# Optimization experiments

Measured on AMD Instinct MI355X. Metric: run time of the kernel, lower is better.

The kernel has to match this reference:

```python
import jax, jax.numpy as jnp
import numpy as np

V, D, NL = 50257, 768, 12
DI, DS, DC, DTR = 1536, 16, 4, 48  # d_inner, d_state, d_conv, dt_rank
B, S = 2, 1024


def _mamba_layer(x, iw, cw, cb, xw, dw, db, Alog, Dp, ow):
    # x: (B,S,D)
    xz = x @ iw.T                      # (B,S,2*DI)
    xin, z = jnp.split(xz, 2, axis=-1)
    # depthwise causal conv over sequence
    xc = jax.lax.conv_general_dilated(
        jnp.transpose(xin, (0, 2, 1)), cw[:, None, :],
        window_strides=(1,), padding=[(DC - 1, 0)],
        feature_group_count=DI, dimension_numbers=('NCL', 'OIL', 'NCL'))
    xin = jax.nn.silu(jnp.transpose(xc, (0, 2, 1)) + cb)  # (B,S,DI)
    dbl = xin @ xw.T                   # (B,S,DTR+2*DS)
    dt, Bm, Cm = dbl[..., :DTR], dbl[..., DTR:DTR + DS], dbl[..., DTR + DS:]
    dt = jax.nn.softplus(dt @ dw.T + db)  # (B,S,DI)
    A = -jnp.exp(Alog)                 # (DI,DS)

    def step(h, inp):
        dt_t, B_t, C_t, x_t = inp      # (B,DI),(B,DS),(B,DS),(B,DI)
        h = h * jnp.exp(dt_t[:, :, None] * A) + (dt_t * x_t)[:, :, None] * B_t[:, None, :]
        y = jnp.einsum('bds,bs->bd', h, C_t)
        return h, y

    h0 = jnp.zeros((x.shape[0], DI, DS), dtype=x.dtype)
    xs = (jnp.transpose(dt, (1, 0, 2)), jnp.transpose(Bm, (1, 0, 2)),
          jnp.transpose(Cm, (1, 0, 2)), jnp.transpose(xin, (1, 0, 2)))
    _, ys = jax.lax.scan(step, h0, xs)
    y = jnp.transpose(ys, (1, 0, 2)) + xin * Dp  # (B,S,DI)
    y = y * jax.nn.silu(z)
    return y @ ow.T                    # (B,S,D)


def _layernorm(x, w, b):
    mu = jnp.mean(x, axis=-1, keepdims=True)
    var = jnp.mean(jnp.square(x - mu), axis=-1, keepdims=True)
    return (x - mu) * jax.lax.rsqrt(var + 1e-5) * w + b


def setup_inputs() -> dict:
    key = jax.random.key(0)
    ks = jax.random.split(key, 10)
    s = 0.02
    input_ids = jax.random.randint(ks[0], (B, S), 0, V)
    emb = jax.random.normal(ks[1], (V, D), jnp.float32) * s
    in_proj_w = jax.random.normal(ks[2], (NL, 2 * DI, D), jnp.float32) * s
    conv_w = jax.random.normal(ks[3], (NL, DI, DC), jnp.float32) * 0.2
    conv_b = jnp.zeros((NL, DI), jnp.float32)
    x_proj_w = jax.random.normal(ks[4], (NL, DTR + 2 * DS, DI), jnp.float32) * s
    dt_proj_w = jax.random.normal(ks[5], (NL, DI, DTR), jnp.float32) * (DTR ** -0.5)
    dt_proj_b = jax.random.normal(ks[6], (NL, DI), jnp.float32) * 0.1 - 4.0
    A_log = jnp.broadcast_to(jnp.log(jnp.arange(1, DS + 1, dtype=jnp.float32)), (NL, DI, DS)) + 0.0
    D_param = jnp.ones((NL, DI), jnp.float32)
    out_proj_w = jax.random.normal(ks[7], (NL, D, DI), jnp.float32) * s
    norm_w = jnp.ones((D,), jnp.float32)
    norm_b = jnp.zeros((D,), jnp.float32)
    return {"input_ids": input_ids, "emb": emb, "in_proj_w": in_proj_w,
            "conv_w": conv_w, "conv_b": conv_b, "x_proj_w": x_proj_w,
            "dt_proj_w": dt_proj_w, "dt_proj_b": dt_proj_b, "A_log": A_log,
            "D_param": D_param, "out_proj_w": out_proj_w,
            "norm_w": norm_w, "norm_b": norm_b}


def reference(input_ids, emb, in_proj_w, conv_w, conv_b, x_proj_w, dt_proj_w,
              dt_proj_b, A_log, D_param, out_proj_w, norm_w, norm_b):
    x = emb[input_ids] * (D ** 0.5)    # (B,S,D)
    for i in range(NL):
        x = _mamba_layer(x, in_proj_w[i], conv_w[i], conv_b[i], x_proj_w[i],
                         dt_proj_w[i], dt_proj_b[i], A_log[i], D_param[i], out_proj_w[i])
    x = _layernorm(x, norm_w, norm_b)
    return x @ emb.T                   # tied lm_head: (B,S,V)
```

## Files before the change

### kernel.cpp

```cpp
#include <hip/hip_runtime.h>
#include <hip/hip_bf16.h>

#define DI 1536
#define DS 16
#define DC 4
#define DTR 48
#define NB 2
#define SL 1024
#define DM 768
#define NLAYER 12
#define VOCAB 50257
#define ROWS (NB*SL)
#define CCH 32
#define CLEN (SL/CCH)
#define NBIG (DI+32)

typedef __attribute__((ext_vector_type(8))) short bf16x8;
typedef __attribute__((ext_vector_type(4))) short short4v;
typedef __attribute__((ext_vector_type(4))) float f32x4;

__device__ inline short f2bf(float f) {
    unsigned u = __builtin_bit_cast(unsigned, f);
    unsigned r = (u + 0x7fffu + ((u >> 16) & 1u)) >> 16;
    return (short)r;
}
__device__ inline float bf2f(unsigned short u) {
    unsigned x = ((unsigned)u) << 16;
    return __builtin_bit_cast(float, x);
}

__device__ __forceinline__ void gl_lds16(const void* g, void* l) {
    __builtin_amdgcn_global_load_lds(
        (const __attribute__((address_space(1))) unsigned int*)g,
        (__attribute__((address_space(3))) unsigned int*)l, 16, 0, 0);
}

__global__ __launch_bounds__(256) void cvt_bf16_k(const float* __restrict__ src,
                                                  unsigned short* __restrict__ dst,
                                                  int n4) {
    int i = blockIdx.x * 256 + threadIdx.x;
    if (i >= n4) return;
    float4 v = *reinterpret_cast<const float4*>(src + (size_t)i * 4);
    short4v o;
    o[0] = f2bf(v.x); o[1] = f2bf(v.y); o[2] = f2bf(v.z); o[3] = f2bf(v.w);
    *reinterpret_cast<short4v*>(dst + (size_t)i * 4) = o;
}

__global__ __launch_bounds__(256) void wc_k(
    const float* __restrict__ dtw_all,
    const float* __restrict__ xpw_all,
    unsigned short* __restrict__ wbig)
{
    int l = blockIdx.z;
    const float* dtw = dtw_all + (size_t)l * DI * DTR;
    const float* xpw = xpw_all + (size_t)l * 80 * DI;
    unsigned short* wb = wbig + (size_t)l * NBIG * DI;
    int tid = threadIdx.x;
    if (blockIdx.y == 12) {
        if (blockIdx.x == 0) {
            for (int idx = tid; idx < 32 * DI; idx += 256) {
                int rr = idx / DI, k = idx - rr * DI;
                wb[(size_t)(DI + rr) * DI + k] =
                    (unsigned short)f2bf(xpw[(size_t)(48 + rr) * DI + k]);
            }
        }
        return;
    }
    __shared__ float sd[128 * 48];
    __shared__ float sx[48 * 128];
    int d0 = blockIdx.y * 128, k0 = blockIdx.x * 128;
    for (int idx = tid; idx < 128 * 48; idx += 256) {
        int r = idx / 48, j = idx - r * 48;
        sd[idx] = dtw[(size_t)(d0 + r) * DTR + j];
    }
    for (int idx = tid; idx < 48 * 128; idx += 256) {
        int j = idx / 128, k = idx - j * 128;
        sx[idx] = xpw[(size_t)j * DI + k0 + k];
    }
    __syncthreads();
    int tx = tid & 15, ty = tid >> 4;
    float acc[8][8] = {};
    for (int j = 0; j < 48; ++j) {
        float a[8], w[8];
        #pragma unroll
        for (int i = 0; i < 8; ++i) a[i] = sd[(ty * 8 + i) * 48 + j];
        #pragma unroll
        for (int i = 0; i < 8; ++i) w[i] = sx[j * 128 + tx * 8 + i];
        #pragma unroll
        for (int i = 0; i < 8; ++i)
            #pragma unroll
            for (int jj = 0; jj < 8; ++jj)
                acc[i][jj] += a[i] * w[jj];
    }
    for (int i = 0; i < 8; ++i)
        for (int jj = 0; jj < 8; ++jj)
            wb[(size_t)(d0 + ty * 8 + i) * DI + k0 + tx * 8 + jj] =
                (unsigned short)f2bf(acc[i][jj]);
}

__global__ __launch_bounds__(256) void embed_k(const int* __restrict__ ids,
                                               const float* __restrict__ emb,
                                               unsigned short* __restrict__ xbf) {
    int i = blockIdx.x * 256 + threadIdx.x;
    if (i >= ROWS * DM) return;
    int row = i / DM;
    int c = i - row * DM;
    xbf[i] = (unsigned short)f2bf(emb[(size_t)ids[row] * DM + c] * 27.712812921102035f);
}

template<int MT, int OUT, bool NTST>
__global__ __launch_bounds__(256) void gemm_bf16(
    const unsigned short* __restrict__ A, int lda,
    const unsigned short* __restrict__ W, int ldw,
    float* __restrict__ C, unsigned short* __restrict__ Cbf, int ldc,
    int GY, int N, int K,
    const float* __restrict__ bias, float* __restrict__ aux)
{
    constexpr int BKT = 32;
    constexpr int CPR = BKT / 8;
    constexpr int ACA = MT * CPR / 256;
    constexpr int ACW = 128 * CPR / 256;
    constexpr int ISS = ACA + ACW;
    constexpr int MFR = MT / 32;
    constexpr int BUFS = (MT + 128) * BKT;
    __shared__ __align__(16) short smem[2 * BUFS];

    const int tid  = threadIdx.x;
    const int lane = tid & 63;
    const int wid  = tid >> 6;
    const int wr   = wid >> 1, wc = wid & 1;

    const int nwg = gridDim.x;
    const int q = nwg >> 3, rm = nwg & 7;
    const int xcd = blockIdx.x & 7, bidx = blockIdx.x >> 3;
    const int wg = (xcd < rm ? xcd * (q + 1) : rm * (q + 1) + (xcd - rm) * q) + bidx;
    const int row0 = (wg % GY) * MT;
    const int col0 = (wg / GY) * 128;

    const unsigned short* gA[ACA];
    const unsigned short* gW[ACW];
    #pragma unroll
    for (int i = 0; i < ACA; ++i) {
        int cid = i * 256 + tid;
        int r = cid / CPR, c = cid % CPR;
        gA[i] = A + (size_t)(row0 + r) * lda + ((c ^ ((r >> 1) & 3)) * 8);
    }
    #pragma unroll
    for (int i = 0; i < ACW; ++i) {
        int cid = i * 256 + tid;
        int r = cid / CPR, c = cid % CPR;
        int rg = col0 + r; if (rg > N - 1) rg = N - 1;
        gW[i] = W + (size_t)rg * ldw + ((c ^ ((r >> 1) & 3)) * 8);
    }

    const int arow = wr * (MT / 2) + (lane & 15);
    const int brow = wc * 64 + (lane & 15);
    const int szA = (arow >> 1) & 3;
    const int szB = (brow >> 1) & 3;
    const int hi = lane >> 4;

    auto STAGE = [&](int buf) {
        short* As = smem + buf * BUFS;
        short* Ws = As + MT * BKT;
        #pragma unroll
        for (int i = 0; i < ACA; ++i) {
            gl_lds16(gA[i], &As[(i * 256 + wid * 64) * 8]);
            gA[i] += BKT;
        }
        #pragma unroll
        for (int i = 0; i < ACW; ++i) {
            gl_lds16(gW[i], &Ws[(i * 256 + wid * 64) * 8]);
            gW[i] += BKT;
        }
    };

    f32x4 acc[MFR][4] = {};

    STAGE(0);
    const int ntiles = K / BKT;
    for (int t = 0; t < ntiles; ++t) {
        const int cur = t & 1;
        if (t + 1 < ntiles) {
            STAGE(cur ^ 1);
            asm volatile("s_waitcnt vmcnt(%0)" :: "n"(ISS) : "memory");
        } else {
            asm volatile("s_waitcnt vmcnt(0)" ::: "memory");
        }
        __builtin_amdgcn_sched_barrier(0);
        __builtin_amdgcn_s_barrier();

        const short* As = smem + cur * BUFS;
        const short* Ws = As + MT * BKT;
        bf16x8 a[MFR], b[4];
        #pragma unroll
        for (int mf = 0; mf < MFR; ++mf)
            a[mf] = *reinterpret_cast<const bf16x8*>(
                &As[(arow + mf * 16) * BKT + ((hi ^ szA) * 8)]);
        #pragma unroll
        for (int nf = 0; nf < 4; ++nf)
            b[nf] = *reinterpret_cast<const bf16x8*>(
                &Ws[(brow + nf * 16) * BKT + ((hi ^ szB) * 8)]);
        #pragma unroll
        for (int mf = 0; mf < MFR; ++mf)
            #pragma unroll
            for (int nf = 0; nf < 4; ++nf)
                acc[mf][nf] = __builtin_amdgcn_mfma_f32_16x16x32_bf16(
                    a[mf], b[nf], acc[mf][nf], 0, 0, 0);

        __builtin_amdgcn_s_barrier();
    }

    if (OUT == 0 && NTST) {
        __syncthreads();
        float* Cs = (float*)smem;
        #pragma unroll
        for (int mf = 0; mf < MFR; ++mf) {
            __syncthreads();
            #pragma unroll
            for (int nf = 0; nf < 4; ++nf) {
                #pragma unroll
                for (int j = 0; j < 4; ++j)
                    Cs[(wr * 16 + hi * 4 + j) * 132 + wc * 64 + nf * 16 + (lane & 15)]
                        = acc[mf][nf][j];
            }
            __syncthreads();
            #pragma unroll
            for (int rr = 0; rr < 8; ++rr) {
                int lrow = wid * 8 + rr;
                int grow = row0 + (lrow < 16 ? mf * 16 + lrow
                                             : (MT / 2) + mf * 16 + (lrow - 16));
                #pragma unroll
                for (int hf = 0; hf < 2; ++hf) {
                    int cc = col0 + hf * 64 + lane;
                    if (cc < N)
                        __builtin_nontemporal_store(
                            Cs[lrow * 132 + hf * 64 + lane],
                            &C[(size_t)grow * ldc + cc]);
                }
            }
        }
    } else {
        #pragma unroll
        for (int mf = 0; mf < MFR; ++mf) {
            #pragma unroll
            for (int nf = 0; nf < 4; ++nf) {
                int r  = row0 + wr * (MT / 2) + mf * 16 + hi * 4;
                int cc = col0 + wc * 64 + nf * 16 + (lane & 15);
                if (cc < N) {
                    f32x4 d = acc[mf][nf];
                    if (OUT == 3) {
                        if (cc < DI) {
                            float bv = bias[cc];
                            #pragma unroll
                            for (int j = 0; j < 4; ++j) {
                                float v = d[j] + bv;
                                v = (v > 20.f) ? v : log1pf(__expf(v));
                                Cbf[(size_t)(r + j) * ldc + cc] = (unsigned short)f2bf(v);
                            }
                        } else {
                            #pragma unroll
                            for (int j = 0; j < 4; ++j)
                                aux[(size_t)(r + j) * 32 + (cc - DI)] = d[j];
                        }
                    } else if (OUT == 2) {
                        #pragma unroll
                        for (int j = 0; j < 4; ++j)
                            Cbf[(size_t)(r + j) * ldc + cc] = (unsigned short)f2bf(d[j]);
                    } else {
                        #pragma unroll
                        for (int j = 0; j < 4; ++j)
                            C[(size_t)(r + j) * ldc + cc] = d[j];
                    }
                }
            }
        }
    }
}

__global__ __launch_bounds__(256) void conv_silu_k(
    const unsigned short* __restrict__ xz, const float* __restrict__ cw,
    const float* __restrict__ cb, unsigned short* __restrict__ xinb)
{
    int i = blockIdx.x * 256 + threadIdx.x;
    if (i >= ROWS * DI) return;
    int row = i / DI;
    int c = i - row * DI;
    int t = row & (SL - 1);
    int b = row >> 10;
    float acc = cb[c];
    const unsigned short* base = xz + (size_t)(b * SL) * (2 * DI) + c;
    #pragma unroll
    for (int k = 0; k < DC; ++k) {
        int tt = t + k - (DC - 1);
        if (tt >= 0) acc += bf2f(base[(size_t)tt * (2 * DI)]) * cw[c * DC + k];
    }
    float v = acc / (1.f + __expf(-acc));
    xinb[i] = (unsigned short)f2bf(v);
}

__global__ __launch_bounds__(256) void scan_phase1(
    const unsigned short* __restrict__ dt,
    const float* __restrict__ bc,
    const unsigned short* __restrict__ xin,
    const float* __restrict__ Alog,
    float* __restrict__ hend,
    float* __restrict__ eprod)
{
    int blk = blockIdx.x;
    int c = blk % CCH;
    int tmp = blk / CCH;
    int dblk = tmp % (DI / 16);
    int b = tmp / (DI / 16);
    int s = threadIdx.x & 15;
    int d = dblk * 16 + (threadIdx.x >> 4);
    float A = -__expf(Alog[d * DS + s]);
    float h = 0.f, P = 1.f;
    const int rowbase = b * SL + c * CLEN;
    #pragma unroll 4
    for (int t = 0; t < CLEN; ++t) {
        int r = rowbase + t;
        float dtv = bf2f(dt[(size_t)r * DI + d]);
        float xv  = bf2f(xin[(size_t)r * DI + d]);
        float Bv  = bc[(size_t)r * 32 + s];
        float e = __expf(dtv * A);
        h = h * e + dtv * xv * Bv;
        P *= e;
    }
    size_t idx = ((size_t)(b * CCH + c) * DI + d) * DS + s;
    hend[idx]  = h;
    eprod[idx] = P;
}

__global__ __launch_bounds__(256) void scan_phase3(
    const unsigned short* __restrict__ dt,
    const float* __restrict__ bc,
    const unsigned short* __restrict__ xin,
    const unsigned short* __restrict__ xz,
    const float* __restrict__ Alog,
    const float* __restrict__ Dp,
    const float* __restrict__ hend,
    const float* __restrict__ eprod,
    unsigned short* __restrict__ ybf)
{
    int blk = blockIdx.x;
    int c = blk % CCH;
    int tmp = blk / CCH;
    int dblk = tmp % (DI / 16);
    int b = tmp / (DI / 16);
    int s = threadIdx.x & 15;
    int d = dblk * 16 + (threadIdx.x >> 4);
    float A = -__expf(Alog[d * DS + s]);
    float Dv = Dp[d];

    float h = 0.f;
    const size_t pbase = ((size_t)b * CCH * DI + d) * DS + s;
    for (int j = 0; j < c; ++j) {
        size_t idx = pbase + (size_t)j * (DI * DS);
        h = h * eprod[idx] + hend[idx];
    }

    const int rowbase = b * SL + c * CLEN;
    #pragma unroll 2
    for (int t = 0; t < CLEN; ++t) {
        int r = rowbase + t;
        float dtv = bf2f(dt[(size_t)r * DI + d]);
        float xv  = bf2f(xin[(size_t)r * DI + d]);
        float Bv  = bc[(size_t)r * 32 + s];
        float Cv  = bc[(size_t)r * 32 + 16 + s];
        float e = __expf(dtv * A);
        h = h * e + dtv * xv * Bv;
        float p = h * Cv;
        p += __shfl_xor(p, 1, 64);
        p += __shfl_xor(p, 2, 64);
        p += __shfl_xor(p, 4, 64);
        p += __shfl_xor(p, 8, 64);
        if (s == 0) {
            float z = bf2f(xz[(size_t)r * (2 * DI) + DI + d]);
            float yv = (p + xv * Dv) * (z / (1.f + __expf(-z)));
            ybf[(size_t)r * DI + d] = (unsigned short)f2bf(yv);
        }
    }
}

__global__ __launch_bounds__(256) void ln_k(
    const unsigned short* __restrict__ x, const float* __restrict__ w,
    const float* __restrict__ b, unsigned short* __restrict__ o)
{
    int row = blockIdx.x;
    int tid = threadIdx.x;
    const unsigned short* xr = x + (size_t)row * DM;
    float v0 = bf2f(xr[tid]), v1 = bf2f(xr[tid + 256]), v2 = bf2f(xr[tid + 512]);
    float s = v0 + v1 + v2;
    #pragma unroll
    for (int off = 1; off < 64; off <<= 1) s += __shfl_xor(s, off, 64);
    __shared__ float red[4];
    __shared__ float red2[4];
    int wid = tid >> 6, lane = tid & 63;
    if (lane == 0) red[wid] = s;
    __syncthreads();
    float mu = (red[0] + red[1] + red[2] + red[3]) * (1.f / 768.f);
    float d0 = v0 - mu, d1 = v1 - mu, d2 = v2 - mu;
    float q = d0 * d0 + d1 * d1 + d2 * d2;
    #pragma unroll
    for (int off = 1; off < 64; off <<= 1) q += __shfl_xor(q, off, 64);
    if (lane == 0) red2[wid] = q;
    __syncthreads();
    float var = (red2[0] + red2[1] + red2[2] + red2[3]) * (1.f / 768.f);
    float rs = rsqrtf(var + 1e-5f);
    o[(size_t)row * DM + tid]       = (unsigned short)f2bf(d0 * rs * w[tid]       + b[tid]);
    o[(size_t)row * DM + tid + 256] = (unsigned short)f2bf(d1 * rs * w[tid + 256] + b[tid + 256]);
    o[(size_t)row * DM + tid + 512] = (unsigned short)f2bf(d2 * rs * w[tid + 512] + b[tid + 512]);
}

extern "C" void kernel_launch(void* const* d_in, const int* in_sizes, int n_in,
                              void* d_out, int out_size, void* d_ws, size_t ws_size,
                              hipStream_t stream) {
    const int*   ids        = (const int*)d_in[0];
    const float* emb        = (const float*)d_in[1];
    const float* in_proj_w  = (const float*)d_in[2];
    const float* conv_w     = (const float*)d_in[3];
    const float* conv_b     = (const float*)d_in[4];
    const float* x_proj_w   = (const float*)d_in[5];
    const float* dt_proj_w  = (const float*)d_in[6];
    const float* dt_proj_b  = (const float*)d_in[7];
    const float* A_log      = (const float*)d_in[8];
    const float* D_param    = (const float*)d_in[9];
    const float* out_proj_w = (const float*)d_in[10];
    const float* norm_w     = (const float*)d_in[11];
    const float* norm_b     = (const float*)d_in[12];
    float* out = (float*)d_out;

    char* base = (char*)d_ws;
    size_t off = 0;
    auto alloc_f = [&](size_t n) { float* p = (float*)(base + off); off += n * 4; return p; };
    auto alloc_u = [&](size_t n) { unsigned short* p = (unsigned short*)(base + off); off += n * 2; return p; };

    float* bc    = alloc_f((size_t)ROWS * 32);
    float* hend  = alloc_f((size_t)NB * CCH * DI * DS);
    float* eprod = alloc_f((size_t)NB * CCH * DI * DS);
    unsigned short* xbf   = alloc_u((size_t)ROWS * DM);
    unsigned short* xzb   = alloc_u((size_t)ROWS * 2 * DI);
    unsigned short* xinb  = alloc_u((size_t)ROWS * DI);
    unsigned short* dtbf  = alloc_u((size_t)ROWS * DI);
    unsigned short* ybf   = alloc_u((size_t)ROWS * DI);
    unsigned short* xlnbf = alloc_u((size_t)ROWS * DM);
    unsigned short* inw_bf = alloc_u((size_t)NLAYER * 2 * DI * DM);
    unsigned short* ow_bf  = alloc_u((size_t)NLAYER * DM * DI);
    unsigned short* wbig  = alloc_u((size_t)NLAYER * NBIG * DI);
    unsigned short* emb_bf = alloc_u((size_t)VOCAB * DM);
    (void)ws_size;

    {
        int n4a = NLAYER * 2 * DI * DM / 4;
        cvt_bf16_k<<<(n4a + 255) / 256, 256, 0, stream>>>(in_proj_w, inw_bf, n4a);
        int n4b = NLAYER * DM * DI / 4;
        cvt_bf16_k<<<(n4b + 255) / 256, 256, 0, stream>>>(out_proj_w, ow_bf, n4b);
        wc_k<<<dim3(12, 13, NLAYER), 256, 0, stream>>>(dt_proj_w, x_proj_w, wbig);
        int n4e = VOCAB * DM / 4;
        cvt_bf16_k<<<(n4e + 255) / 256, 256, 0, stream>>>(emb, emb_bf, n4e);
    }

    embed_k<<<(ROWS * DM + 255) / 256, 256, 0, stream>>>(ids, emb, xbf);

    const int scan_grid = NB * (DI / 16) * CCH;

    for (int i = 0; i < NLAYER; ++i) {
        const float* cw  = conv_w  + (size_t)i * DI * DC;
        const float* cb  = conv_b  + (size_t)i * DI;
        const float* dtb = dt_proj_b + (size_t)i * DI;
        const float* Al  = A_log   + (size_t)i * DI * DS;
        const float* Dpar= D_param + (size_t)i * DI;

        const unsigned short* inw = inw_bf + (size_t)i * 2 * DI * DM;
        gemm_bf16<64, 2, false><<<24 * 32, 256, 0, stream>>>(
            xbf, DM, inw, DM, nullptr, xzb, 2 * DI, 32, 2 * DI, DM, nullptr, nullptr);

        conv_silu_k<<<(ROWS * DI) / 256, 256, 0, stream>>>(xzb, cw, cb, xinb);

        const unsigned short* wb = wbig + (size_t)i * NBIG * DI;
        gemm_bf16<64, 3, false><<<13 * 32, 256, 0, stream>>>(
            xinb, DI, wb, DI, nullptr, dtbf, DI, 32, NBIG, DI, dtb, bc);

        scan_phase1<<<scan_grid, 256, 0, stream>>>(dtbf, bc, xinb, Al, hend, eprod);
        scan_phase3<<<scan_grid, 256, 0, stream>>>(dtbf, bc, xinb, xzb, Al, Dpar,
                                                   hend, eprod, ybf);

        const unsigned short* ow = ow_bf + (size_t)i * DM * DI;
        gemm_bf16<64, 2, false><<<6 * 32, 256, 0, stream>>>(
            ybf, DI, ow, DI, nullptr, xbf, DM, 32, DM, DI, nullptr, nullptr);
    }

    ln_k<<<ROWS, 256, 0, stream>>>(xbf, norm_w, norm_b, xlnbf);
    gemm_bf16<128, 0, true><<<393 * 16, 256, 0, stream>>>(
        xlnbf, DM, emb_bf, DM, out, nullptr, VOCAB, 16, VOCAB, DM, nullptr, nullptr);
}
```

Baseline: 3.204 ms.

## Triple-buffer GEMM loads, add 32-row tile for out_proj, vectorize conv and embed

The GEMM template gains a buffer-count parameter. The per-layer GEMMs now use three shared-memory stages with matching vmcnt waits, so global loads are issued two tiles ahead. The out_proj GEMM switches to a 32-row tile with a 384-block grid to fill more CUs. The conv+SiLU and embedding kernels are vectorized to process 8 and 4 elements per thread with wide loads and stores. The cost is more LDS use per block, and the MT=32 staging path needs special-cased indexing that could be fragile.

```diff
diff --git a/kernel.cpp b/kernel.cpp
--- a/kernel.cpp
+++ b/kernel.cpp
@@ -102,13 +102,19 @@
                                                const float* __restrict__ emb,
                                                unsigned short* __restrict__ xbf) {
     int i = blockIdx.x * 256 + threadIdx.x;
-    if (i >= ROWS * DM) return;
-    int row = i / DM;
-    int c = i - row * DM;
-    xbf[i] = (unsigned short)f2bf(emb[(size_t)ids[row] * DM + c] * 27.712812921102035f);
-}
-
-template<int MT, int OUT, bool NTST>
+    if (i >= ROWS * (DM / 4)) return;
+    int row = i / (DM / 4);
+    int c4 = (i - row * (DM / 4)) * 4;
+    float4 v = *reinterpret_cast<const float4*>(
+        &emb[(size_t)ids[row] * DM + c4]);
+    const float s = 27.712812921102035f;
+    short4v o;
+    o[0] = f2bf(v.x * s); o[1] = f2bf(v.y * s);
+    o[2] = f2bf(v.z * s); o[3] = f2bf(v.w * s);
+    *reinterpret_cast<short4v*>(&xbf[(size_t)row * DM + c4]) = o;
+}
+
+template<int MT, int NBUF, int OUT, bool NTST>
 __global__ __launch_bounds__(256) void gemm_bf16(
     const unsigned short* __restrict__ A, int lda,
     const unsigned short* __restrict__ W, int ldw,
@@ -118,12 +124,12 @@
 {
     constexpr int BKT = 32;
     constexpr int CPR = BKT / 8;
-    constexpr int ACA = MT * CPR / 256;
+    constexpr int ACA = (MT * CPR + 255) / 256;
     constexpr int ACW = 128 * CPR / 256;
     constexpr int ISS = ACA + ACW;
     constexpr int MFR = MT / 32;
     constexpr int BUFS = (MT + 128) * BKT;
-    __shared__ __align__(16) short smem[2 * BUFS];
+    __shared__ __align__(16) short smem[NBUF * BUFS];
 
     const int tid  = threadIdx.x;
     const int lane = tid & 63;
@@ -141,7 +147,7 @@
     const unsigned short* gW[ACW];
     #pragma unroll
     for (int i = 0; i < ACA; ++i) {
-        int cid = i * 256 + tid;
+        int cid = i * 256 + ((MT == 32) ? (tid & 127) : tid);
         int r = cid / CPR, c = cid % CPR;
         gA[i] = A + (size_t)(row0 + r) * lda + ((c ^ ((r >> 1) & 3)) * 8);
     }
@@ -153,7 +159,7 @@
         gW[i] = W + (size_t)rg * ldw + ((c ^ ((r >> 1) & 3)) * 8);
     }
 
-    const int arow = wr * (MT / 2) + (lane & 15);
+    const int arow = (MT == 32 ? wr * 16 : wr * (MT / 2)) + (lane & 15);
     const int brow = wc * 64 + (lane & 15);
     const int szA = (arow >> 1) & 3;
     const int szB = (brow >> 1) & 3;
@@ -164,7 +170,8 @@
         short* Ws = As + MT * BKT;
         #pragma unroll
         for (int i = 0; i < ACA; ++i) {
-            gl_lds16(gA[i], &As[(i * 256 + wid * 64) * 8]);
+            int cbase = (MT == 32) ? ((wid & 1) * 64) : (i * 256 + wid * 64);
+            gl_lds16(gA[i], &As[cbase * 8]);
             gA[i] += BKT;
         }
         #pragma unroll
@@ -176,20 +183,25 @@
 
     f32x4 acc[MFR][4] = {};
 
-    STAGE(0);
     const int ntiles = K / BKT;
+    #pragma unroll
+    for (int p = 0; p < NBUF - 1; ++p) STAGE(p);
+
     for (int t = 0; t < ntiles; ++t) {
-        const int cur = t & 1;
-        if (t + 1 < ntiles) {
-            STAGE(cur ^ 1);
+        const int next = t + NBUF - 1;
+        if (next < ntiles) STAGE(next % NBUF);
+        int ahead = ntiles - 1 - t;
+        if (ahead > NBUF - 1) ahead = NBUF - 1;
+        if (NBUF == 3 && ahead == 2)
+            asm volatile("s_waitcnt vmcnt(%0)" :: "n"(2 * ISS) : "memory");
+        else if (ahead == 1)
             asm volatile("s_waitcnt vmcnt(%0)" :: "n"(ISS) : "memory");
-        } else {
+        else if (ahead == 0)
             asm volatile("s_waitcnt vmcnt(0)" ::: "memory");
-        }
         __builtin_amdgcn_sched_barrier(0);
         __builtin_amdgcn_s_barrier();
 
-        const short* As = smem + cur * BUFS;
+        const short* As = smem + (t % NBUF) * BUFS;
         const short* Ws = As + MT * BKT;
         bf16x8 a[MFR], b[4];
         #pragma unroll
@@ -244,7 +256,7 @@
         for (int mf = 0; mf < MFR; ++mf) {
             #pragma unroll
             for (int nf = 0; nf < 4; ++nf) {
-                int r  = row0 + wr * (MT / 2) + mf * 16 + hi * 4;
+                int r  = row0 + (MT == 32 ? wr * 16 : wr * (MT / 2)) + mf * 16 + hi * 4;
                 int cc = col0 + wc * 64 + nf * 16 + (lane & 15);
                 if (cc < N) {
                     f32x4 d = acc[mf][nf];
@@ -282,20 +294,39 @@
     const float* __restrict__ cb, unsigned short* __restrict__ xinb)
 {
     int i = blockIdx.x * 256 + threadIdx.x;
-    if (i >= ROWS * DI) return;
-    int row = i / DI;
-    int c = i - row * DI;
+    if (i >= ROWS * (DI / 8)) return;
+    int row = i / (DI / 8);
+    int c = (i - row * (DI / 8)) * 8;
     int t = row & (SL - 1);
     int b = row >> 10;
-    float acc = cb[c];
-    const unsigned short* base = xz + (size_t)(b * SL) * (2 * DI) + c;
+
+    float4 wv[8];
+    float accv[8];
+    #pragma unroll
+    for (int j = 0; j < 8; ++j) {
+        wv[j] = *reinterpret_cast<const float4*>(&cw[(c + j) * DC]);
+        accv[j] = cb[c + j];
+    }
+    const unsigned short* base = xz + ((size_t)(b * SL)) * (2 * DI) + c;
     #pragma unroll
     for (int k = 0; k < DC; ++k) {
         int tt = t + k - (DC - 1);
-        if (tt >= 0) acc += bf2f(base[(size_t)tt * (2 * DI)]) * cw[c * DC + k];
-    }
-    float v = acc / (1.f + __expf(-acc));
-    xinb[i] = (unsigned short)f2bf(v);
+        if (tt >= 0) {
+            bf16x8 v = *reinterpret_cast<const bf16x8*>(
+                &base[(size_t)tt * (2 * DI)]);
+            #pragma unroll
+            for (int j = 0; j < 8; ++j)
+                accv[j] += bf2f((unsigned short)v[j]) *
+                           reinterpret_cast<const float*>(&wv[j])[k];
+        }
+    }
+    bf16x8 o;
+    #pragma unroll
+    for (int j = 0; j < 8; ++j) {
+        float v = accv[j] / (1.f + __expf(-accv[j]));
+        o[j] = f2bf(v);
+    }
+    *reinterpret_cast<bf16x8*>(&xinb[(size_t)row * DI + c]) = o;
 }
 
 __global__ __launch_bounds__(256) void scan_phase1(
@@ -460,7 +491,7 @@
         cvt_bf16_k<<<(n4e + 255) / 256, 256, 0, stream>>>(emb, emb_bf, n4e);
     }
 
-    embed_k<<<(ROWS * DM + 255) / 256, 256, 0, stream>>>(ids, emb, xbf);
+    embed_k<<<(ROWS * (DM / 4) + 255) / 256, 256, 0, stream>>>(ids, emb, xbf);
 
     const int scan_grid = NB * (DI / 16) * CCH;
 
@@ -472,13 +503,13 @@
         const float* Dpar= D_param + (size_t)i * DI;
 
         const unsigned short* inw = inw_bf + (size_t)i * 2 * DI * DM;
-        gemm_bf16<64, 2, false><<<24 * 32, 256, 0, stream>>>(
+        gemm_bf16<64, 3, 2, false><<<24 * 32, 256, 0, stream>>>(
             xbf, DM, inw, DM, nullptr, xzb, 2 * DI, 32, 2 * DI, DM, nullptr, nullptr);
 
-        conv_silu_k<<<(ROWS * DI) / 256, 256, 0, stream>>>(xzb, cw, cb, xinb);
+        conv_silu_k<<<(ROWS * (DI / 8)) / 256, 256, 0, stream>>>(xzb, cw, cb, xinb);
 
         const unsigned short* wb = wbig + (size_t)i * NBIG * DI;
-        gemm_bf16<64, 3, false><<<13 * 32, 256, 0, stream>>>(
+        gemm_bf16<64, 3, 3, false><<<13 * 32, 256, 0, stream>>>(
             xinb, DI, wb, DI, nullptr, dtbf, DI, 32, NBIG, DI, dtb, bc);
 
         scan_phase1<<<scan_grid, 256, 0, stream>>>(dtbf, bc, xinb, Al, hend, eprod);
@@ -486,11 +517,11 @@
                                                    hend, eprod, ybf);
 
         const unsigned short* ow = ow_bf + (size_t)i * DM * DI;
-        gemm_bf16<64, 2, false><<<6 * 32, 256, 0, stream>>>(
-            ybf, DI, ow, DI, nullptr, xbf, DM, 32, DM, DI, nullptr, nullptr);
+        gemm_bf16<32, 3, 2, false><<<64 * 6, 256, 0, stream>>>(
+            ybf, DI, ow, DI, nullptr, xbf, DM, 64, DM, DI, nullptr, nullptr);
     }
 
     ln_k<<<ROWS, 256, 0, stream>>>(xbf, norm_w, norm_b, xlnbf);
-    gemm_bf16<128, 0, true><<<393 * 16, 256, 0, stream>>>(
+    gemm_bf16<128, 2, 0, true><<<393 * 16, 256, 0, stream>>>(
         xlnbf, DM, emb_bf, DM, out, nullptr, VOCAB, 16, VOCAB, DM, nullptr, nullptr);
 }
```

Result: faster. 3.130 ms (-2.3%).
